# Optimization experiments

Hardware: AMD Instinct MI355X
Metric: run time of the kernel (lower is better)

## Reference

```python
import jax, jax.numpy as jnp
import numpy as np

NEG_INF = -1e10


def setup_inputs() -> dict:
    key = jax.random.key(0)
    ks = jax.random.split(key, 9)
    B, S, H, E = 64, 4096, 512, 512
    hidden = jax.random.normal(ks[0], (B, H), dtype=jnp.float32)
    encoder_outputs = jax.random.normal(ks[1], (B, S, E), dtype=jnp.float32)
    mask = jax.random.randint(ks[2], (B, S), 0, 2, dtype=jnp.int32)
    s = 1.0 / np.sqrt(H)
    Wq = jax.random.uniform(ks[3], (H, H), jnp.float32, -s, s)
    bq = jax.random.uniform(ks[4], (H,), jnp.float32, -s, s)
    se = 1.0 / np.sqrt(E)
    Wk = jax.random.uniform(ks[5], (E, H), jnp.float32, -se, se)
    bk = jax.random.uniform(ks[6], (H,), jnp.float32, -se, se)
    Wv = jax.random.uniform(ks[7], (H, 1), jnp.float32, -s, s)
    bv = jax.random.uniform(ks[8], (1,), jnp.float32, -s, s)
    return {"hidden": hidden, "encoder_outputs": encoder_outputs, "mask": mask,
            "Wq": Wq, "bq": bq, "Wk": Wk, "bk": bk, "Wv": Wv, "bv": bv}


def reference(hidden, encoder_outputs, mask, Wq, bq, Wk, bk, Wv, bv):
    # query projection: (B, H) -> broadcast over src_len
    q = hidden @ Wq + bq                       # (B, H)
    k = jnp.einsum('bse,eh->bsh', encoder_outputs, Wk) + bk  # (B, S, H)
    energy = jnp.tanh(q[:, None, :] + k)       # (B, S, H)
    scores = jnp.einsum('bsh,h->bs', energy, Wv[:, 0]) + bv[0]  # (B, S)
    scores = jnp.where(mask == 0, NEG_INF, scores)
    attn = jax.nn.softmax(scores, axis=1)      # (B, S)
    context = jnp.einsum('bs,bse->be', attn, encoder_outputs)   # (B, E)
    return context, attn
```

## Files before the change

### kernel.cpp

```cpp
#include <hip/hip_runtime.h>
#include <hip/hip_bf16.h>

#define B_ 64
#define S_ 4096
#define H_ 512
#define E_ 512
#define NEG_INF_ -1e10f

typedef __attribute__((ext_vector_type(8))) short short8;
typedef __attribute__((ext_vector_type(16))) float f32x16;

static __device__ __forceinline__ unsigned short f2bf(float f) {
    union { float f; unsigned u; } v; v.f = f;
    unsigned x = v.u;
    x += 0x7FFFu + ((x >> 16) & 1u);
    return (unsigned short)(x >> 16);
}

static __device__ __forceinline__ unsigned pk2(float lo, float hi) {
    float2 f; f.x = lo; f.y = hi;
    union { __hip_bfloat162 h; unsigned u; } c;
    c.h = __float22bfloat162_rn(f);
    return c.u;
}

static __device__ __forceinline__ void gload_lds16(const void* g, void* l) {
    __builtin_amdgcn_global_load_lds(
        (const __attribute__((address_space(1))) void*)g,
        (__attribute__((address_space(3))) void*)l, 16, 0, 0);
}

__global__ void prep_wkt(const float* __restrict__ wk, unsigned short* __restrict__ wkt) {
    int idx = blockIdx.x * 256 + threadIdx.x;
    int h = idx >> 9, e = idx & 511;
    wkt[idx] = f2bf(wk[e * H_ + h]);
}

__global__ void prep_qb(const float* __restrict__ hidden, const float* __restrict__ wq,
                        const float* __restrict__ bq, const float* __restrict__ bk,
                        float* __restrict__ qb) {
    __shared__ float hid[H_];
    int b = blockIdx.x, t = threadIdx.x;
    hid[t]       = hidden[b * H_ + t];
    hid[t + 256] = hidden[b * H_ + t + 256];
    __syncthreads();
    for (int hh = t; hh < H_; hh += 256) {
        float s = 0.f;
        for (int e = 0; e < H_; ++e) s += hid[e] * wq[e * H_ + hh];
        qb[b * H_ + hh] = s + bq[hh] + bk[hh];
    }
}

__global__ __launch_bounds__(256, 3) void scores_kernel(
    const float* __restrict__ enc, const unsigned short* __restrict__ wkt,
    const float* __restrict__ qb, const float* __restrict__ wv,
    float* __restrict__ part)
{
    __shared__ char lds[38912];

    int id = blockIdx.x;
    int xcd = id & 7, qq = id >> 3;
    int logical = xcd * 1024 + qq;
    int b  = logical >> 7;
    int r  = logical & 127;
    int st = r >> 2, nt = r & 3;
    int s0 = st * 128;

    const int tid  = threadIdx.x;
    const int lane = tid & 63;
    const int wave = tid >> 6;
    const int wr   = wave >> 1;
    const int wc   = wave & 1;
    const int l31  = lane & 31;
    const int g    = lane >> 5;

    const float* encb = enc + ((size_t)b * S_ + s0) * E_;

    auto loadA = [&](int kc, float4 (&rg)[8]) {
#pragma unroll
        for (int j = 0; j < 2; ++j) {
            int sid = tid * 2 + j;
            int row = sid >> 2, ksl = sid & 3;
            const float* pr = encb + (size_t)row * 512 + kc * 64 + ksl * 8;
#pragma unroll
            for (int kk = 0; kk < 2; ++kk) {
                rg[j * 4 + kk * 2 + 0] = *(const float4*)(pr + kk * 32);
                rg[j * 4 + kk * 2 + 1] = *(const float4*)(pr + kk * 32 + 4);
            }
        }
    };
    auto writeA = [&](const float4 (&rg)[8]) {
#pragma unroll
        for (int j = 0; j < 2; ++j) {
            int sid = tid * 2 + j;
            int row = sid >> 2, ksl = sid & 3;
            int srow = row & 31;
            int sst  = ((row >> 5) * 4 + ksl) ^ (srow & 15);
#pragma unroll
            for (int kk = 0; kk < 2; ++kk) {
                const float4& a = rg[j * 4 + kk * 2 + 0];
                const float4& c = rg[j * 4 + kk * 2 + 1];
                union { short8 s; unsigned u[4]; } u;
                u.u[0] = pk2(a.x, a.y); u.u[1] = pk2(a.z, a.w);
                u.u[2] = pk2(c.x, c.y); u.u[3] = pk2(c.z, c.w);
                *(short8*)(lds + kk * 8192 + srow * 256 + sst * 16) = u.s;
            }
        }
    };
    auto stageB = [&](int kc) {
#pragma unroll
        for (int kk = 0; kk < 2; ++kk) {
            char* buf = lds + 16384 + kk * 8192;
#pragma unroll
            for (int p = 0; p < 2; ++p) {
                int gi0 = p * 256 + wave * 64;
                char* db = buf + gi0 * 16;
                int gi = gi0 + lane;
                int sn = gi >> 4, ss = gi & 15;
                int sl = ss ^ (sn & 15);
                int n  = (sl >> 2) * 32 + sn;
                const unsigned short* gp =
                    wkt + (size_t)(nt * 128 + n) * 512 + kc * 64 + kk * 32 + (sl & 3) * 8;
                gload_lds16(gp, db);
            }
        }
    };

    f32x16 acc[2][2];
#pragma unroll
    for (int mr = 0; mr < 2; ++mr)
#pragma unroll
        for (int nf = 0; nf < 2; ++nf)
#pragma unroll
            for (int e = 0; e < 16; ++e) acc[mr][nf][e] = 0.f;

    float4 ar[8];
    loadA(0, ar);

    for (int kc = 0; kc < 8; ++kc) {
        __syncthreads();
        writeA(ar);
        stageB(kc);
        __syncthreads();
        if (kc < 7) loadA(kc + 1, ar);
        const char* Ap = lds;
        const char* Bp = lds + 16384;
#pragma unroll
        for (int kst = 0; kst < 4; ++kst) {
            const int kk = kst >> 1, ks = kst & 1;
            short8 af[2], bf[2];
#pragma unroll
            for (int mr = 0; mr < 2; ++mr) {
                int sl = (wr * 2 + mr) * 4 + ks * 2 + g;
                af[mr] = *(const short8*)(Ap + kk * 8192 + l31 * 256 + ((sl ^ (l31 & 15)) << 4));
            }
#pragma unroll
            for (int nf = 0; nf < 2; ++nf) {
                int sl = (wc * 2 + nf) * 4 + ks * 2 + g;
                bf[nf] = *(const short8*)(Bp + kk * 8192 + l31 * 256 + ((sl ^ (l31 & 15)) << 4));
            }
            acc[0][0] = __builtin_amdgcn_mfma_f32_32x32x16_bf16(af[0], bf[0], acc[0][0], 0, 0, 0);
            acc[0][1] = __builtin_amdgcn_mfma_f32_32x32x16_bf16(af[0], bf[1], acc[0][1], 0, 0, 0);
            acc[1][0] = __builtin_amdgcn_mfma_f32_32x32x16_bf16(af[1], bf[0], acc[1][0], 0, 0, 0);
            acc[1][1] = __builtin_amdgcn_mfma_f32_32x32x16_bf16(af[1], bf[1], acc[1][1], 0, 0, 0);
        }
    }

    float p[2][16];
#pragma unroll
    for (int nf = 0; nf < 2; ++nf) {
        int col = nt * 128 + wc * 64 + nf * 32 + l31;
        float qv  = qb[b * H_ + col];
        float wvv = wv[col];
#pragma unroll
        for (int mr = 0; mr < 2; ++mr)
#pragma unroll
            for (int e = 0; e < 16; ++e) {
                float x  = qv + acc[mr][nf][e];
                float ex = __expf(2.f * x);
                float th = 1.f - 2.f / (ex + 1.f);
                float v  = wvv * th;
                p[mr][e] = nf ? (p[mr][e] + v) : v;
            }
    }

    __syncthreads();
    float* ps = (float*)lds;
#pragma unroll
    for (int mr = 0; mr < 2; ++mr)
#pragma unroll
        for (int e = 0; e < 16; ++e) {
            int row = mr * 32 + (e & 3) + 8 * (e >> 2) + 4 * g;
            ps[(wave * 64 + row) * 36 + l31] = p[mr][e];
        }
    __syncthreads();
    float rsum = 0.f;
    {
        const float* myrow = ps + (size_t)(wave * 64 + lane) * 36;
#pragma unroll
        for (int j = 0; j < 8; ++j) {
            float4 v = *(const float4*)(myrow + j * 4);
            rsum += (v.x + v.y) + (v.z + v.w);
        }
    }
    float* pf = (float*)(lds + 36864);
    pf[wave * 64 + lane] = rsum;
    __syncthreads();
    if (tid < 128) {
        int wr2 = tid >> 6, rr = tid & 63;
        float v = pf[(wr2 * 2 + 0) * 64 + rr] + pf[(wr2 * 2 + 1) * 64 + rr];
        int s = s0 + wr2 * 64 + rr;
        part[((size_t)b * S_ + s) * 4 + nt] = v;
    }
}

__global__ void softmax_kernel(const float* __restrict__ part, const int* __restrict__ mask,
                               const float* __restrict__ bvp, float* __restrict__ attn) {
    __shared__ float red[8];
    int b = blockIdx.x, tid = threadIdx.x;
    int wid = tid >> 6, lane = tid & 63;
    float bv0 = bvp[0];
    float vals[8];
    float mx = -3.4e38f;
#pragma unroll
    for (int i = 0; i < 8; ++i) {
        int s = i * 512 + tid;
        float4 v = *(const float4*)(part + ((size_t)b * S_ + s) * 4);
        float sc = (v.x + v.y) + (v.z + v.w) + bv0;
        sc = mask[(size_t)b * S_ + s] ? sc : NEG_INF_;
        vals[i] = sc;
        mx = fmaxf(mx, sc);
    }
#pragma unroll
    for (int off = 1; off < 64; off <<= 1) mx = fmaxf(mx, __shfl_xor(mx, off));
    if (lane == 0) red[wid] = mx;
    __syncthreads();
    mx = red[0];
#pragma unroll
    for (int w = 1; w < 8; ++w) mx = fmaxf(mx, red[w]);
    __syncthreads();
    float sum = 0.f;
#pragma unroll
    for (int i = 0; i < 8; ++i) { vals[i] = __expf(vals[i] - mx); sum += vals[i]; }
#pragma unroll
    for (int off = 1; off < 64; off <<= 1) sum += __shfl_xor(sum, off);
    if (lane == 0) red[wid] = sum;
    __syncthreads();
    sum = red[0] + red[1] + red[2] + red[3] + red[4] + red[5] + red[6] + red[7];
    float inv = 1.f / sum;
#pragma unroll
    for (int i = 0; i < 8; ++i) attn[(size_t)b * S_ + i * 512 + tid] = vals[i] * inv;
}

__global__ void ctx_partial(const float* __restrict__ attn, const float* __restrict__ enc,
                            float* __restrict__ part) {
    __shared__ float a[256];
    int c = blockIdx.x, b = blockIdx.y, t = threadIdx.x;
    a[t] = attn[(size_t)b * S_ + c * 256 + t];
    __syncthreads();
    const float* ep = enc + (size_t)b * S_ * E_ + (size_t)c * 256 * E_ + t * 2;
    float x = 0.f, y = 0.f;
#pragma unroll 4
    for (int s = 0; s < 256; ++s) {
        float2 v = *(const float2*)(ep + (size_t)s * E_);
        x += a[s] * v.x;
        y += a[s] * v.y;
    }
    float* o = part + ((size_t)c * B_ + b) * E_ + t * 2;
    o[0] = x; o[1] = y;
}

__global__ void ctx_reduce(const float* __restrict__ part, float* __restrict__ ctx) {
    int idx = blockIdx.x * 256 + threadIdx.x;
    float s = 0.f;
#pragma unroll
    for (int c = 0; c < 16; ++c) s += part[(size_t)c * (B_ * E_) + idx];
    ctx[idx] = s;
}

extern "C" void kernel_launch(void* const* d_in, const int* in_sizes, int n_in,
                              void* d_out, int out_size, void* d_ws, size_t ws_size,
                              hipStream_t stream) {
    const float* hidden = (const float*)d_in[0];
    const float* enc    = (const float*)d_in[1];
    const int*   mask   = (const int*)d_in[2];
    const float* Wq     = (const float*)d_in[3];
    const float* bq     = (const float*)d_in[4];
    const float* Wk     = (const float*)d_in[5];
    const float* bk     = (const float*)d_in[6];
    const float* Wv     = (const float*)d_in[7];
    const float* bv     = (const float*)d_in[8];

    float* out  = (float*)d_out;
    char*  ws   = (char*)d_ws;
    float*          qbuf   = (float*)ws;
    unsigned short* wkt    = (unsigned short*)(ws + 131072);
    float*          pscore = (float*)(ws + 655360);
    float*          cpart  = (float*)(ws + 655360);

    float* ctx  = out;
    float* attn = out + B_ * E_;

    prep_wkt<<<1024, 256, 0, stream>>>(Wk, wkt);
    prep_qb<<<64, 256, 0, stream>>>(hidden, Wq, bq, bk, qbuf);
    scores_kernel<<<8192, 256, 0, stream>>>(enc, wkt, qbuf, Wv, pscore);
    softmax_kernel<<<64, 512, 0, stream>>>(pscore, mask, bv, attn);
    ctx_partial<<<dim3(16, 64), 256, 0, stream>>>(attn, enc, cpart);
    ctx_reduce<<<128, 256, 0, stream>>>(cpart, ctx);
}
```

Before: 421.7 us.

## Enlarge scores tile to 256 rows with 8 waves sharing each Wk tile

The scores GEMM block grows from 128 to 256 sequence rows and from 4 to 8 waves, with each block still covering 128 hidden columns. The LDS layout is reorganised so the A tile holds two 128-row halves per k-chunk. The epilogue reduction is rewritten to accumulate the two column-wave partials in LDS. This halves the number of times each Wk tile is staged per row and the grid size, at the cost of more LDS per block (48KB) and a tighter register budget from the 512-thread launch bound, which may cut occupancy.

```diff
diff --git a/kernel.cpp b/kernel.cpp
--- a/kernel.cpp
+++ b/kernel.cpp
@@ -51,20 +51,20 @@
     }
 }
 
-__global__ __launch_bounds__(256, 3) void scores_kernel(
+__global__ __launch_bounds__(512, 6) void scores_kernel(
     const float* __restrict__ enc, const unsigned short* __restrict__ wkt,
     const float* __restrict__ qb, const float* __restrict__ wv,
     float* __restrict__ part)
 {
-    __shared__ char lds[38912];
+    __shared__ char lds[49152];
 
     int id = blockIdx.x;
     int xcd = id & 7, qq = id >> 3;
-    int logical = xcd * 1024 + qq;
-    int b  = logical >> 7;
-    int r  = logical & 127;
+    int logical = xcd * 512 + qq;
+    int b  = logical >> 6;
+    int r  = logical & 63;
     int st = r >> 2, nt = r & 3;
-    int s0 = st * 128;
+    int s0 = st * 256;
 
     const int tid  = threadIdx.x;
     const int lane = tid & 63;
@@ -78,51 +78,43 @@
 
     auto loadA = [&](int kc, float4 (&rg)[8]) {
 #pragma unroll
-        for (int j = 0; j < 2; ++j) {
-            int sid = tid * 2 + j;
-            int row = sid >> 2, ksl = sid & 3;
-            const float* pr = encb + (size_t)row * 512 + kc * 64 + ksl * 8;
-#pragma unroll
-            for (int kk = 0; kk < 2; ++kk) {
-                rg[j * 4 + kk * 2 + 0] = *(const float4*)(pr + kk * 32);
-                rg[j * 4 + kk * 2 + 1] = *(const float4*)(pr + kk * 32 + 4);
-            }
+        for (int j = 0; j < 4; ++j) {
+            int c = tid * 4 + j;
+            int row = c >> 3, ksl = c & 7;
+            const float* p = encb + (size_t)row * 512 + kc * 64 + ksl * 8;
+            rg[j * 2 + 0] = *(const float4*)p;
+            rg[j * 2 + 1] = *(const float4*)(p + 4);
         }
     };
     auto writeA = [&](const float4 (&rg)[8]) {
 #pragma unroll
-        for (int j = 0; j < 2; ++j) {
-            int sid = tid * 2 + j;
-            int row = sid >> 2, ksl = sid & 3;
-            int srow = row & 31;
-            int sst  = ((row >> 5) * 4 + ksl) ^ (srow & 15);
-#pragma unroll
-            for (int kk = 0; kk < 2; ++kk) {
-                const float4& a = rg[j * 4 + kk * 2 + 0];
-                const float4& c = rg[j * 4 + kk * 2 + 1];
-                union { short8 s; unsigned u[4]; } u;
-                u.u[0] = pk2(a.x, a.y); u.u[1] = pk2(a.z, a.w);
-                u.u[2] = pk2(c.x, c.y); u.u[3] = pk2(c.z, c.w);
-                *(short8*)(lds + kk * 8192 + srow * 256 + sst * 16) = u.s;
-            }
+        for (int j = 0; j < 4; ++j) {
+            int c = tid * 4 + j;
+            int row = c >> 3, ksl = c & 7;
+            int kk = ksl >> 2, k2 = ksl & 3;
+            int half = row >> 7, r7 = row & 127, srow = r7 & 31;
+            int sst = (((r7 >> 5) * 4 + k2)) ^ (srow & 15);
+            union { short8 s; unsigned u[4]; } u;
+            u.u[0] = pk2(rg[j * 2].x, rg[j * 2].y);
+            u.u[1] = pk2(rg[j * 2].z, rg[j * 2].w);
+            u.u[2] = pk2(rg[j * 2 + 1].x, rg[j * 2 + 1].y);
+            u.u[3] = pk2(rg[j * 2 + 1].z, rg[j * 2 + 1].w);
+            *(short8*)(lds + kk * 16384 + half * 8192 + srow * 256 + sst * 16) = u.s;
         }
     };
     auto stageB = [&](int kc) {
 #pragma unroll
         for (int kk = 0; kk < 2; ++kk) {
-            char* buf = lds + 16384 + kk * 8192;
-#pragma unroll
-            for (int p = 0; p < 2; ++p) {
-                int gi0 = p * 256 + wave * 64;
-                char* db = buf + gi0 * 16;
-                int gi = gi0 + lane;
-                int sn = gi >> 4, ss = gi & 15;
-                int sl = ss ^ (sn & 15);
-                int n  = (sl >> 2) * 32 + sn;
-                const unsigned short* gp =
-                    wkt + (size_t)(nt * 128 + n) * 512 + kc * 64 + kk * 32 + (sl & 3) * 8;
-                gload_lds16(gp, db);
-            }
+            char* buf = lds + 32768 + kk * 8192;
+            int gi0 = wave * 64;
+            char* db = buf + gi0 * 16;
+            int gi = gi0 + lane;
+            int sn = gi >> 4, ss = gi & 15;
+            int sl = ss ^ (sn & 15);
+            int n  = (sl >> 2) * 32 + sn;
+            const unsigned short* gp =
+                wkt + (size_t)(nt * 128 + n) * 512 + kc * 64 + kk * 32 + (sl & 3) * 8;
+            gload_lds16(gp, db);
         }
     };
 
@@ -143,21 +135,23 @@
         stageB(kc);
         __syncthreads();
         if (kc < 7) loadA(kc + 1, ar);
-        const char* Ap = lds;
-        const char* Bp = lds + 16384;
 #pragma unroll
         for (int kst = 0; kst < 4; ++kst) {
             const int kk = kst >> 1, ks = kst & 1;
             short8 af[2], bf[2];
 #pragma unroll
             for (int mr = 0; mr < 2; ++mr) {
-                int sl = (wr * 2 + mr) * 4 + ks * 2 + g;
-                af[mr] = *(const short8*)(Ap + kk * 8192 + l31 * 256 + ((sl ^ (l31 & 15)) << 4));
+                int idxm = wr * 2 + mr;
+                int halfA = idxm >> 2, qr = idxm & 3;
+                int sl = qr * 4 + ks * 2 + g;
+                af[mr] = *(const short8*)(lds + kk * 16384 + halfA * 8192 +
+                                          l31 * 256 + ((sl ^ (l31 & 15)) << 4));
             }
 #pragma unroll
             for (int nf = 0; nf < 2; ++nf) {
                 int sl = (wc * 2 + nf) * 4 + ks * 2 + g;
-                bf[nf] = *(const short8*)(Bp + kk * 8192 + l31 * 256 + ((sl ^ (l31 & 15)) << 4));
+                bf[nf] = *(const short8*)(lds + 32768 + kk * 8192 +
+                                          l31 * 256 + ((sl ^ (l31 & 15)) << 4));
             }
             acc[0][0] = __builtin_amdgcn_mfma_f32_32x32x16_bf16(af[0], bf[0], acc[0][0], 0, 0, 0);
             acc[0][1] = __builtin_amdgcn_mfma_f32_32x32x16_bf16(af[0], bf[1], acc[0][1], 0, 0, 0);
@@ -184,33 +178,46 @@
             }
     }
 
-    __syncthreads();
     float* ps = (float*)lds;
-#pragma unroll
-    for (int mr = 0; mr < 2; ++mr)
-#pragma unroll
-        for (int e = 0; e < 16; ++e) {
-            int row = mr * 32 + (e & 3) + 8 * (e >> 2) + 4 * g;
-            ps[(wave * 64 + row) * 36 + l31] = p[mr][e];
-        }
-    __syncthreads();
-    float rsum = 0.f;
+    __syncthreads();
+    if (wc == 0) {
+#pragma unroll
+        for (int mr = 0; mr < 2; ++mr)
+#pragma unroll
+            for (int e = 0; e < 16; ++e) {
+                int row = wr * 64 + mr * 32 + (e & 3) + 8 * (e >> 2) + 4 * g;
+                ps[row * 37 + l31] = p[mr][e];
+            }
+    }
+    __syncthreads();
+    if (wc == 1) {
+#pragma unroll
+        for (int mr = 0; mr < 2; ++mr)
+#pragma unroll
+            for (int e = 0; e < 16; ++e) {
+                int row = wr * 64 + mr * 32 + (e & 3) + 8 * (e >> 2) + 4 * g;
+                ps[row * 37 + l31] += p[mr][e];
+            }
+    }
+    __syncthreads();
     {
-        const float* myrow = ps + (size_t)(wave * 64 + lane) * 36;
-#pragma unroll
-        for (int j = 0; j < 8; ++j) {
+        int rr   = tid & 255;
+        int half = tid >> 8;
+        const float* myrow = ps + rr * 37 + half * 16;
+        float rsum = 0.f;
+#pragma unroll
+        for (int j = 0; j < 4; ++j) {
             float4 v = *(const float4*)(myrow + j * 4);
             rsum += (v.x + v.y) + (v.z + v.w);
         }
-    }
-    float* pf = (float*)(lds + 36864);
-    pf[wave * 64 + lane] = rsum;
-    __syncthreads();
-    if (tid < 128) {
-        int wr2 = tid >> 6, rr = tid & 63;
-        float v = pf[(wr2 * 2 + 0) * 64 + rr] + pf[(wr2 * 2 + 1) * 64 + rr];
-        int s = s0 + wr2 * 64 + rr;
-        part[((size_t)b * S_ + s) * 4 + nt] = v;
+        float* pf = (float*)(lds + 37888);
+        pf[half * 256 + rr] = rsum;
+    }
+    __syncthreads();
+    if (tid < 256) {
+        float* pf = (float*)(lds + 37888);
+        float v = pf[tid] + pf[256 + tid];
+        part[((size_t)b * S_ + s0 + tid) * 4 + nt] = v;
     }
 }
 
@@ -303,7 +310,7 @@
 
     prep_wkt<<<1024, 256, 0, stream>>>(Wk, wkt);
     prep_qb<<<64, 256, 0, stream>>>(hidden, Wq, bq, bk, qbuf);
-    scores_kernel<<<8192, 256, 0, stream>>>(enc, wkt, qbuf, Wv, pscore);
+    scores_kernel<<<4096, 512, 0, stream>>>(enc, wkt, qbuf, Wv, pscore);
     softmax_kernel<<<64, 512, 0, stream>>>(pscore, mask, bv, attn);
     ctx_partial<<<dim3(16, 64), 256, 0, stream>>>(attn, enc, cpart);
     ctx_reduce<<<128, 256, 0, stream>>>(cpart, ctx);
```

Measured after the change: 1.480 ms. 251% more time.
